# Performance work log

Measured on AMD Instinct MI355X. Metric: run time of the kernel, lower is better.

## Reference

```python
import jax, jax.numpy as jnp
import numpy as np

B, V = 256, 128000
NOISE_MIN = 1e-10


def setup_inputs() -> dict:
    key = jax.random.key(0)
    k_log, k_temp, k_noise = jax.random.split(key, 3)
    logits = jax.random.normal(k_log, (B, V), dtype=jnp.float32)
    temperatures = jax.random.uniform(k_temp, (B,), dtype=jnp.float32)
    # first quarter of rows use greedy decoding (temperature <= 0)
    temperatures = temperatures.at[: B // 4].set(0.0)
    # torch's empty_like().exponential_(1) -> Exp(1) noise, passed explicitly for determinism
    noise = jax.random.exponential(k_noise, (B, V), dtype=jnp.float32)
    return {"logits": logits, "temperatures": temperatures, "noise": noise}


def reference(logits, temperatures, noise):
    logits = logits.astype(jnp.float32)  # [B, V]
    greedy = temperatures <= 0           # [B]
    # avoid div-by-zero on greedy rows; their result is overwritten by jnp.where below
    safe_t = jnp.where(greedy, 1.0, temperatures)
    probs = jax.nn.softmax(logits / safe_t[:, None], axis=-1)          # [B, V]
    sampled_tok = jnp.argmax(probs / jnp.maximum(noise, NOISE_MIN), axis=-1)  # Gumbel-style sampling
    greedy_tok = jnp.argmax(logits, axis=-1)
    return jnp.where(greedy, greedy_tok, sampled_tok).astype(jnp.int64)
```

## Files before the change

kernel.cpp:

```cpp
#include <hip/hip_runtime.h>
#include <math.h>

#define B 256
#define V 128000
#define VVEC (V / 4)
#define NOISE_MIN 1e-10f
#define BLOCK 1024

__device__ __forceinline__ void upd(float v, int i, float& bv, int& bi) {
    if (v > bv || (v == bv && i < bi)) { bv = v; bi = i; }
}

__global__ __launch_bounds__(BLOCK) void sampler_kernel(
    const float* __restrict__ logits,
    const float* __restrict__ temps,
    const float* __restrict__ noise,
    int* __restrict__ out)
{
    const int row = blockIdx.x;
    const float t = temps[row];
    const bool greedy = (t <= 0.0f);
    const float invT = greedy ? 1.0f : (1.0f / t);

    const size_t base = (size_t)row * V;
    const float4* __restrict__ lg = reinterpret_cast<const float4*>(logits + base);
    const float4* __restrict__ nz = reinterpret_cast<const float4*>(noise + base);

    float bestVal = -INFINITY;
    int   bestIdx = 0x7FFFFFFF;

    if (greedy) {
        for (int v = threadIdx.x; v < VVEC; v += BLOCK) {
            float4 l = lg[v];
            int i0 = v << 2;
            upd(l.x, i0 + 0, bestVal, bestIdx);
            upd(l.y, i0 + 1, bestVal, bestIdx);
            upd(l.z, i0 + 2, bestVal, bestIdx);
            upd(l.w, i0 + 3, bestVal, bestIdx);
        }
    } else {
        for (int v = threadIdx.x; v < VVEC; v += BLOCK) {
            float4 l = lg[v];
            float4 n = nz[v];
            int i0 = v << 2;
            float kx = l.x * invT - __logf(fmaxf(n.x, NOISE_MIN));
            float ky = l.y * invT - __logf(fmaxf(n.y, NOISE_MIN));
            float kz = l.z * invT - __logf(fmaxf(n.z, NOISE_MIN));
            float kw = l.w * invT - __logf(fmaxf(n.w, NOISE_MIN));
            upd(kx, i0 + 0, bestVal, bestIdx);
            upd(ky, i0 + 1, bestVal, bestIdx);
            upd(kz, i0 + 2, bestVal, bestIdx);
            upd(kw, i0 + 3, bestVal, bestIdx);
        }
    }

    #pragma unroll
    for (int off = 32; off > 0; off >>= 1) {
        float ov = __shfl_down(bestVal, off, 64);
        int   oi = __shfl_down(bestIdx, off, 64);
        if (ov > bestVal || (ov == bestVal && oi < bestIdx)) { bestVal = ov; bestIdx = oi; }
    }

    __shared__ float sVal[BLOCK / 64];
    __shared__ int   sIdx[BLOCK / 64];
    const int wave = threadIdx.x >> 6;
    const int lane = threadIdx.x & 63;
    if (lane == 0) { sVal[wave] = bestVal; sIdx[wave] = bestIdx; }
    __syncthreads();

    if (wave == 0) {
        const int nw = BLOCK / 64;
        bestVal = (lane < nw) ? sVal[lane] : -INFINITY;
        bestIdx = (lane < nw) ? sIdx[lane] : 0x7FFFFFFF;
        #pragma unroll
        for (int off = 8; off > 0; off >>= 1) {
            float ov = __shfl_down(bestVal, off, 64);
            int   oi = __shfl_down(bestIdx, off, 64);
            if (ov > bestVal || (ov == bestVal && oi < bestIdx)) { bestVal = ov; bestIdx = oi; }
        }
        if (lane == 0) out[row] = bestIdx;
    }
}

extern "C" void kernel_launch(void* const* d_in, const int* in_sizes, int n_in,
                              void* d_out, int out_size, void* d_ws, size_t ws_size,
                              hipStream_t stream) {
    const float* logits = (const float*)d_in[0];
    const float* temps  = (const float*)d_in[1];
    const float* noise  = (const float*)d_in[2];
    int* out = (int*)d_out;

    sampler_kernel<<<B, BLOCK, 0, stream>>>(logits, temps, noise, out);
}
```

Baseline: 269.7 us.

## Split each row across chunked blocks with packed-key argmax and second reduce kernel

Each row is now split into 8 chunks handled by separate 256-thread blocks, so there are 2048 blocks instead of 256. The per-row partial maxima are combined by a small second kernel. Value and index are packed into one sortable 64-bit key so the shuffle reductions use a single max, and the main loop is unrolled by two with dual accumulators to keep more loads in flight. The cost is an extra kernel launch and a dependency on workspace memory for the partial results.

```diff
diff --git a/kernel.cpp b/kernel.cpp
--- a/kernel.cpp
+++ b/kernel.cpp
@@ -3,21 +3,31 @@
 
 #define B 256
 #define V 128000
+#define NOISE_MIN 1e-10f
+#define CHUNKS 8
+#define BLOCK 256
 #define VVEC (V / 4)
-#define NOISE_MIN 1e-10f
-#define BLOCK 1024
+#define CVEC (VVEC / CHUNKS)
 
 __device__ __forceinline__ void upd(float v, int i, float& bv, int& bi) {
     if (v > bv || (v == bv && i < bi)) { bv = v; bi = i; }
 }
 
-__global__ __launch_bounds__(BLOCK) void sampler_kernel(
+__device__ __forceinline__ unsigned long long packKey(float v, int i) {
+    unsigned int b = __float_as_uint(v);
+    unsigned int u = (b & 0x80000000u) ? ~b : (b | 0x80000000u);
+    return ((unsigned long long)u << 32) | (unsigned int)(~i);
+}
+
+__global__ __launch_bounds__(BLOCK, 8) void partial_kernel(
     const float* __restrict__ logits,
     const float* __restrict__ temps,
     const float* __restrict__ noise,
-    int* __restrict__ out)
+    unsigned long long* __restrict__ partials)
 {
-    const int row = blockIdx.x;
+    const int row   = blockIdx.x / CHUNKS;
+    const int chunk = blockIdx.x % CHUNKS;
+
     const float t = temps[row];
     const bool greedy = (t <= 0.0f);
     const float invT = greedy ? 1.0f : (1.0f / t);
@@ -26,59 +36,110 @@
     const float4* __restrict__ lg = reinterpret_cast<const float4*>(logits + base);
     const float4* __restrict__ nz = reinterpret_cast<const float4*>(noise + base);
 
-    float bestVal = -INFINITY;
-    int   bestIdx = 0x7FFFFFFF;
+    const int start = chunk * CVEC;
+    const int end   = start + CVEC;
 
+    float bv0 = -INFINITY, bv1 = -INFINITY;
+    int   bi0 = 0x7FFFFFFF, bi1 = 0x7FFFFFFF;
+
+    int v = start + threadIdx.x;
     if (greedy) {
-        for (int v = threadIdx.x; v < VVEC; v += BLOCK) {
-            float4 l = lg[v];
-            int i0 = v << 2;
-            upd(l.x, i0 + 0, bestVal, bestIdx);
-            upd(l.y, i0 + 1, bestVal, bestIdx);
-            upd(l.z, i0 + 2, bestVal, bestIdx);
-            upd(l.w, i0 + 3, bestVal, bestIdx);
+        for (; v + BLOCK < end; v += 2 * BLOCK) {
+            float4 a = lg[v];
+            float4 b = lg[v + BLOCK];
+            int ia = v << 2, ib = (v + BLOCK) << 2;
+            upd(a.x, ia + 0, bv0, bi0);
+            upd(a.y, ia + 1, bv0, bi0);
+            upd(a.z, ia + 2, bv0, bi0);
+            upd(a.w, ia + 3, bv0, bi0);
+            upd(b.x, ib + 0, bv1, bi1);
+            upd(b.y, ib + 1, bv1, bi1);
+            upd(b.z, ib + 2, bv1, bi1);
+            upd(b.w, ib + 3, bv1, bi1);
+        }
+        if (v < end) {
+            float4 a = lg[v];
+            int ia = v << 2;
+            upd(a.x, ia + 0, bv0, bi0);
+            upd(a.y, ia + 1, bv0, bi0);
+            upd(a.z, ia + 2, bv0, bi0);
+            upd(a.w, ia + 3, bv0, bi0);
         }
     } else {
-        for (int v = threadIdx.x; v < VVEC; v += BLOCK) {
-            float4 l = lg[v];
-            float4 n = nz[v];
-            int i0 = v << 2;
-            float kx = l.x * invT - __logf(fmaxf(n.x, NOISE_MIN));
-            float ky = l.y * invT - __logf(fmaxf(n.y, NOISE_MIN));
-            float kz = l.z * invT - __logf(fmaxf(n.z, NOISE_MIN));
-            float kw = l.w * invT - __logf(fmaxf(n.w, NOISE_MIN));
-            upd(kx, i0 + 0, bestVal, bestIdx);
-            upd(ky, i0 + 1, bestVal, bestIdx);
-            upd(kz, i0 + 2, bestVal, bestIdx);
-            upd(kw, i0 + 3, bestVal, bestIdx);
+        for (; v + BLOCK < end; v += 2 * BLOCK) {
+            float4 la = lg[v];
+            float4 na = nz[v];
+            float4 lb = lg[v + BLOCK];
+            float4 nb = nz[v + BLOCK];
+            int ia = v << 2, ib = (v + BLOCK) << 2;
+            float kax = la.x * invT - __logf(fmaxf(na.x, NOISE_MIN));
+            float kay = la.y * invT - __logf(fmaxf(na.y, NOISE_MIN));
+            float kaz = la.z * invT - __logf(fmaxf(na.z, NOISE_MIN));
+            float kaw = la.w * invT - __logf(fmaxf(na.w, NOISE_MIN));
+            float kbx = lb.x * invT - __logf(fmaxf(nb.x, NOISE_MIN));
+            float kby = lb.y * invT - __logf(fmaxf(nb.y, NOISE_MIN));
+            float kbz = lb.z * invT - __logf(fmaxf(nb.z, NOISE_MIN));
+            float kbw = lb.w * invT - __logf(fmaxf(nb.w, NOISE_MIN));
+            upd(kax, ia + 0, bv0, bi0);
+            upd(kay, ia + 1, bv0, bi0);
+            upd(kaz, ia + 2, bv0, bi0);
+            upd(kaw, ia + 3, bv0, bi0);
+            upd(kbx, ib + 0, bv1, bi1);
+            upd(kby, ib + 1, bv1, bi1);
+            upd(kbz, ib + 2, bv1, bi1);
+            upd(kbw, ib + 3, bv1, bi1);
+        }
+        if (v < end) {
+            float4 la = lg[v];
+            float4 na = nz[v];
+            int ia = v << 2;
+            float kax = la.x * invT - __logf(fmaxf(na.x, NOISE_MIN));
+            float kay = la.y * invT - __logf(fmaxf(na.y, NOISE_MIN));
+            float kaz = la.z * invT - __logf(fmaxf(na.z, NOISE_MIN));
+            float kaw = la.w * invT - __logf(fmaxf(na.w, NOISE_MIN));
+            upd(kax, ia + 0, bv0, bi0);
+            upd(kay, ia + 1, bv0, bi0);
+            upd(kaz, ia + 2, bv0, bi0);
+            upd(kaw, ia + 3, bv0, bi0);
         }
     }
 
+    if (bv1 > bv0 || (bv1 == bv0 && bi1 < bi0)) { bv0 = bv1; bi0 = bi1; }
+
+    unsigned long long key = packKey(bv0, bi0);
     #pragma unroll
     for (int off = 32; off > 0; off >>= 1) {
-        float ov = __shfl_down(bestVal, off, 64);
-        int   oi = __shfl_down(bestIdx, off, 64);
-        if (ov > bestVal || (ov == bestVal && oi < bestIdx)) { bestVal = ov; bestIdx = oi; }
+        unsigned long long o = __shfl_down(key, off, 64);
+        key = (o > key) ? o : key;
     }
 
-    __shared__ float sVal[BLOCK / 64];
-    __shared__ int   sIdx[BLOCK / 64];
+    __shared__ unsigned long long sKey[BLOCK / 64];
     const int wave = threadIdx.x >> 6;
     const int lane = threadIdx.x & 63;
-    if (lane == 0) { sVal[wave] = bestVal; sIdx[wave] = bestIdx; }
+    if (lane == 0) sKey[wave] = key;
     __syncthreads();
 
-    if (wave == 0) {
-        const int nw = BLOCK / 64;
-        bestVal = (lane < nw) ? sVal[lane] : -INFINITY;
-        bestIdx = (lane < nw) ? sIdx[lane] : 0x7FFFFFFF;
+    if (threadIdx.x == 0) {
+        unsigned long long k = sKey[0];
         #pragma unroll
-        for (int off = 8; off > 0; off >>= 1) {
-            float ov = __shfl_down(bestVal, off, 64);
-            int   oi = __shfl_down(bestIdx, off, 64);
-            if (ov > bestVal || (ov == bestVal && oi < bestIdx)) { bestVal = ov; bestIdx = oi; }
+        for (int w = 1; w < BLOCK / 64; ++w)
+            k = (sKey[w] > k) ? sKey[w] : k;
+        partials[blockIdx.x] = k;
+    }
+}
+
+__global__ void reduce_kernel(const unsigned long long* __restrict__ partials,
+                              int* __restrict__ out)
+{
+    const int row = blockIdx.x * blockDim.x + threadIdx.x;
+    if (row < B) {
+        unsigned long long k = partials[(size_t)row * CHUNKS];
+        #pragma unroll
+        for (int c = 1; c < CHUNKS; ++c) {
+            unsigned long long o = partials[(size_t)row * CHUNKS + c];
+            k = (o > k) ? o : k;
         }
-        if (lane == 0) out[row] = bestIdx;
+        out[row] = (int)(~(unsigned int)k);
     }
 }
 
@@ -90,5 +151,8 @@
     const float* noise  = (const float*)d_in[2];
     int* out = (int*)d_out;
 
-    sampler_kernel<<<B, BLOCK, 0, stream>>>(logits, temps, noise, out);
+    unsigned long long* partials = (unsigned long long*)d_ws;
+
+    partial_kernel<<<B * CHUNKS, BLOCK, 0, stream>>>(logits, temps, noise, partials);
+    reduce_kernel<<<1, B, 0, stream>>>(partials, out);
 }
```

New measurement: 270.4 us. About the same (+0.3%).
